# Kernel optimization log

Measured on AMD Instinct MI355X. Metric: run time of the kernel, lower is better.

The kernel has to match this reference:

```python
import jax, jax.numpy as jnp
import numpy as np

L = 16384          # leaves of complete binary tree
D = 256            # word_dim == tree_input_dim == output_dim
V = 50257          # num_words
NL = 5             # num_labels


def setup_inputs() -> dict:
    key = jax.random.key(0)
    ks = jax.random.split(key, 8)
    s = 0.05
    return {
        "tokens": jax.random.randint(ks[0], (L,), 0, V),
        "emb": jax.random.normal(ks[1], (V, D), jnp.float32) * s,      # word_embedding.weight
        "Wx": jax.random.normal(ks[2], (D, 5 * D), jnp.float32) * s,   # input->gates (leaf only)
        "Ul": jax.random.normal(ks[3], (D, 5 * D), jnp.float32) * s,   # left-child h -> gates
        "Ur": jax.random.normal(ks[4], (D, 5 * D), jnp.float32) * s,   # right-child h -> gates
        "b": jnp.zeros((5 * D,), jnp.float32),
        "Wp": jax.random.normal(ks[5], (D, NL), jnp.float32) * s,      # pred_layer
        "bp": jnp.zeros((NL,), jnp.float32),
    }


def _cell(pre, c_l, c_r):
    # Binary TreeLSTM cell: gates [i, f_l, f_r, o, u]
    i, fl, fr, o, u = jnp.split(pre, 5, axis=-1)
    c = jax.nn.sigmoid(i) * jnp.tanh(u) + jax.nn.sigmoid(fl) * c_l + jax.nn.sigmoid(fr) * c_r
    h = jax.nn.sigmoid(o) * jnp.tanh(c)
    return h, c


def reference(tokens, emb, Wx, Ul, Ur, b, Wp, bp):
    # dropout layers are identity at inference (no-op here)
    x = emb[tokens]                                  # [L, D] seq_output == word embeddings (leaf_rnn=False)
    # leaf nodes: l/r child states are zeros, inputs = seq_out[idx]
    h, c = _cell(x @ Wx + b, 0.0, 0.0)               # [L, D]
    hs = [h]
    # internal nodes level by level (complete binary tree): inputs=None -> no Wx term
    while h.shape[0] > 1:
        hl, hr = h[0::2], h[1::2]
        cl, cr = c[0::2], c[1::2]
        h, c = _cell(hl @ Ul + hr @ Ur + b, cl, cr)
        hs.append(h)
    hidden = jnp.concatenate(hs, axis=0)             # [2L-1, D] all node hidden states
    return hidden @ Wp + bp                          # single_h_pred logits [2L-1, NL]
```

## Files before the change

kernel.cpp:

```cpp
#include <hip/hip_runtime.h>
#include <hip/hip_bf16.h>
#include <math.h>
#include <stdint.h>


typedef __attribute__((ext_vector_type(8))) short     bf16x8;
typedef __attribute__((ext_vector_type(4))) float     f32x4;
typedef __attribute__((ext_vector_type(8))) unsigned short u16x8;

#define NGATE 5

__device__ __forceinline__ uint16_t f2bf(float f) {
    uint32_t u = __builtin_bit_cast(uint32_t, f);
    u = (u + 0x7fffu + ((u >> 16) & 1u)) >> 16;
    return (uint16_t)u;
}
__device__ __forceinline__ float bf2f(uint16_t h) {
    uint32_t u = ((uint32_t)h) << 16;
    return __builtin_bit_cast(float, u);
}
__device__ __forceinline__ float sigf(float x) { return 1.0f / (1.0f + __expf(-x)); }
__device__ __forceinline__ float tanhfast(float x) {
    float e = __expf(2.0f * x);
    return (e - 1.0f) / (e + 1.0f);
}

__device__ __forceinline__ void gld_lds16(const void* g, void* l) {
    __builtin_amdgcn_global_load_lds(
        (const __attribute__((address_space(1))) void*)g,
        (__attribute__((address_space(3))) void*)l,
        16, 0, 0);
}

__global__ __launch_bounds__(256) void pack_w_kernel(
    const float* __restrict__ W0, const float* __restrict__ W1, int KT,
    uint16_t* __restrict__ dhi, uint16_t* __restrict__ dlo)
{
    int gid = blockIdx.x * 256 + threadIdx.x;
    int total = 80 * KT * 64;
    if (gid >= total) return;
    int lane = gid & 63;
    int n  = ((gid >> 6) / KT) * 16 + (lane & 15);
    int kt = (gid >> 6) % KT;
    int k0 = kt * 32 + (lane >> 4) * 8;
    u16x8 vh, vl;
    #pragma unroll
    for (int j = 0; j < 8; ++j) {
        int k = k0 + j;
        const float* src = (k < 256) ? (W0 + (size_t)k * 1280)
                                     : (W1 + (size_t)(k - 256) * 1280);
        float v = src[n];
        uint16_t h = f2bf(v);
        vh[j] = h;
        vl[j] = f2bf(v - bf2f(h));
    }
    *(u16x8*)(dhi + (size_t)gid * 8) = vh;
    *(u16x8*)(dlo + (size_t)gid * 8) = vl;
}

template<int BM, int KT, bool LVL0>
__global__ __launch_bounds__(256) void lvl_gemm(
    const uint16_t* __restrict__ Ahi, const uint16_t* __restrict__ Alo,
    const int* __restrict__ tokens, const float* __restrict__ emb,
    const uint16_t* __restrict__ Bhi, const uint16_t* __restrict__ Blo,
    const float* __restrict__ b,
    const float* __restrict__ c_prev,
    uint16_t* __restrict__ h_hi_out, uint16_t* __restrict__ h_lo_out,
    float* __restrict__ c_out, int n)
{
    constexpr int K   = KT * 32;
    constexpr int MT  = BM / 64;
    constexpr int ACH = BM / 16;

    __shared__ __align__(16) uint16_t lA[2][BM * 32];
    __shared__ __align__(16) uint16_t lB[NGATE * 2 * 512];

    const int tid  = threadIdx.x;
    const int wave = tid >> 6;
    const int lane = tid & 63;
    const int quad = lane >> 4;
    const int l15  = lane & 15;
    const int r0   = blockIdx.x * BM;
    const int jn   = blockIdx.y;

    f32x4 acc[MT][NGATE] = {};

    for (int kt = 0; kt < KT; ++kt) {
        if (!LVL0) {
            for (int c = wave; c < 2 * ACH; c += 4) {
                int mat = (c >= ACH) ? 1 : 0;
                int ci  = mat ? (c - ACH) : c;
                const uint16_t* src = mat ? Alo : Ahi;
                int row = r0 + ci * 16 + (lane >> 2);
                row = min(row, n - 1);
                const uint16_t* g = src + (size_t)row * K + kt * 32 + (lane & 3) * 8;
                gld_lds16(g, &lA[mat][ci * 512]);
            }
        } else {
            int row = tid >> 1, kh = tid & 1;
            int tok = tokens[r0 + row];
            const float* src = emb + (size_t)tok * 256 + kt * 32 + kh * 16;
            float v[16];
            #pragma unroll
            for (int q = 0; q < 4; ++q) {
                float4 f = *(const float4*)(src + 4 * q);
                v[4*q] = f.x; v[4*q+1] = f.y; v[4*q+2] = f.z; v[4*q+3] = f.w;
            }
            u16x8 h0, h1, l0, l1;
            #pragma unroll
            for (int j = 0; j < 8; ++j) {
                uint16_t h = f2bf(v[j]);     h0[j] = h; l0[j] = f2bf(v[j]     - bf2f(h));
                uint16_t g = f2bf(v[j + 8]); h1[j] = g; l1[j] = f2bf(v[j + 8] - bf2f(g));
            }
            int o = row * 32 + kh * 16;
            *(u16x8*)&lA[0][o]     = h0;  *(u16x8*)&lA[0][o + 8] = h1;
            *(u16x8*)&lA[1][o]     = l0;  *(u16x8*)&lA[1][o + 8] = l1;
        }
        for (int c = wave; c < 2 * NGATE; c += 4) {
            int g  = c >> 1, hl = c & 1;
            const uint16_t* src = hl ? Blo : Bhi;
            int nt = g * 16 + jn;
            const uint16_t* gp = src + ((size_t)(nt * KT + kt) * 64 + lane) * 8;
            gld_lds16(gp, &lB[(g * 2 + hl) * 512]);
        }
        __syncthreads();

        bf16x8 a_hi[MT], a_lo[MT];
        #pragma unroll
        for (int mt = 0; mt < MT; ++mt) {
            int row = wave * (BM / 4) + mt * 16 + l15;
            a_hi[mt] = *(const bf16x8*)&lA[0][row * 32 + quad * 8];
            a_lo[mt] = *(const bf16x8*)&lA[1][row * 32 + quad * 8];
        }
        #pragma unroll
        for (int g = 0; g < NGATE; ++g) {
            bf16x8 bh = *(const bf16x8*)&lB[(g * 2 + 0) * 512 + lane * 8];
            bf16x8 bl = *(const bf16x8*)&lB[(g * 2 + 1) * 512 + lane * 8];
            #pragma unroll
            for (int mt = 0; mt < MT; ++mt) {
                acc[mt][g] = __builtin_amdgcn_mfma_f32_16x16x32_bf16(a_hi[mt], bh, acc[mt][g], 0, 0, 0);
                acc[mt][g] = __builtin_amdgcn_mfma_f32_16x16x32_bf16(a_lo[mt], bh, acc[mt][g], 0, 0, 0);
                acc[mt][g] = __builtin_amdgcn_mfma_f32_16x16x32_bf16(a_hi[mt], bl, acc[mt][g], 0, 0, 0);
            }
        }
        __syncthreads();
    }

    const int d = jn * 16 + l15;
    float bg[NGATE];
    #pragma unroll
    for (int g = 0; g < NGATE; ++g) bg[g] = b[g * 256 + d];

    #pragma unroll
    for (int mt = 0; mt < MT; ++mt) {
        int rb = r0 + wave * (BM / 4) + mt * 16 + quad * 4;
        #pragma unroll
        for (int v = 0; v < 4; ++v) {
            int row = rb + v;
            if (row < n) {
                float gi = acc[mt][0][v] + bg[0];
                float fl = acc[mt][1][v] + bg[1];
                float fr = acc[mt][2][v] + bg[2];
                float go = acc[mt][3][v] + bg[3];
                float gu = acc[mt][4][v] + bg[4];
                float cc;
                if (LVL0) {
                    cc = sigf(gi) * tanhfast(gu);
                } else {
                    float cl = c_prev[(size_t)(2 * row) * 256 + d];
                    float cr = c_prev[(size_t)(2 * row + 1) * 256 + d];
                    cc = sigf(gi) * tanhfast(gu) + sigf(fl) * cl + sigf(fr) * cr;
                }
                float hh = sigf(go) * tanhfast(cc);
                uint16_t hb = f2bf(hh);
                h_hi_out[(size_t)row * 256 + d] = hb;
                h_lo_out[(size_t)row * 256 + d] = f2bf(hh - bf2f(hb));
                c_out[(size_t)row * 256 + d] = cc;
            }
        }
    }
}

__global__ __launch_bounds__(256) void proj_kernel(
    const uint16_t* __restrict__ h_hi, const uint16_t* __restrict__ h_lo,
    const float* __restrict__ Wp, const float* __restrict__ bp,
    float* __restrict__ out, int n)
{
    const int wave = blockIdx.x * 4 + (threadIdx.x >> 6);
    const int lane = threadIdx.x & 63;
    if (wave >= n) return;

    const uint16_t* hh = h_hi + (size_t)wave * 256;
    const uint16_t* hl = h_lo + (size_t)wave * 256;
    float s[5] = {0.f, 0.f, 0.f, 0.f, 0.f};
    #pragma unroll
    for (int q = 0; q < 4; ++q) {
        int dd = lane + 64 * q;
        float hv = bf2f(hh[dd]) + bf2f(hl[dd]);
        #pragma unroll
        for (int j = 0; j < 5; ++j) s[j] += hv * Wp[dd * 5 + j];
    }
    #pragma unroll
    for (int off = 32; off; off >>= 1)
        #pragma unroll
        for (int j = 0; j < 5; ++j) s[j] += __shfl_down(s[j], off);

    if (lane == 0) {
        #pragma unroll
        for (int j = 0; j < 5; ++j) out[(size_t)wave * 5 + j] = s[j] + bp[j];
    }
}

extern "C" void kernel_launch(void* const* d_in, const int* in_sizes, int n_in,
                              void* d_out, int out_size, void* d_ws, size_t ws_size,
                              hipStream_t stream)
{
    const int*   tokens = (const int*)  d_in[0];
    const float* emb    = (const float*)d_in[1];
    const float* Wx     = (const float*)d_in[2];
    const float* Ul     = (const float*)d_in[3];
    const float* Ur     = (const float*)d_in[4];
    const float* b      = (const float*)d_in[5];
    const float* Wp     = (const float*)d_in[6];
    const float* bp     = (const float*)d_in[7];
    float* out = (float*)d_out;

    uint8_t* w = (uint8_t*)d_ws;
    uint16_t* h_hi = (uint16_t*)w;  w += (size_t)32767 * 256 * 2;
    uint16_t* h_lo = (uint16_t*)w;  w += (size_t)32767 * 256 * 2;
    float*    cA   = (float*)w;     w += (size_t)16384 * 256 * 4;
    float*    cB   = (float*)w;     w += (size_t)8192  * 256 * 4;
    uint16_t* BxH  = (uint16_t*)w;  w += (size_t)80 * 8  * 64 * 8 * 2;
    uint16_t* BxL  = (uint16_t*)w;  w += (size_t)80 * 8  * 64 * 8 * 2;
    uint16_t* BuH  = (uint16_t*)w;  w += (size_t)80 * 16 * 64 * 8 * 2;
    uint16_t* BuL  = (uint16_t*)w;  w += (size_t)80 * 16 * 64 * 8 * 2;

    pack_w_kernel<<<(80 * 8  * 64) / 256, 256, 0, stream>>>(Wx, Wx, 8,  BxH, BxL);
    pack_w_kernel<<<(80 * 16 * 64) / 256, 256, 0, stream>>>(Ul, Ur, 16, BuH, BuL);

    int off[16];
    off[0] = 0;
    for (int t = 0; t < 15; ++t) off[t + 1] = off[t] + (16384 >> t);

    lvl_gemm<128, 8, true><<<dim3(16384 / 128, 16), 256, 0, stream>>>(
        nullptr, nullptr, tokens, emb, BxH, BxL, b, nullptr,
        h_hi, h_lo, cA, 16384);

    for (int t = 1; t <= 14; ++t) {
        int n = 16384 >> t;
        const uint16_t* Ah = h_hi + (size_t)off[t - 1] * 256;
        const uint16_t* Al = h_lo + (size_t)off[t - 1] * 256;
        float* c_in  = (t % 2 == 0) ? cB : cA;
        float* c_out = (t % 2 == 0) ? cA : cB;
        uint16_t* Hh = h_hi + (size_t)off[t] * 256;
        uint16_t* Hl = h_lo + (size_t)off[t] * 256;
        if (n >= 4096) {
            lvl_gemm<128, 16, false><<<dim3(n / 128, 16), 256, 0, stream>>>(
                Ah, Al, nullptr, nullptr, BuH, BuL, b, c_in, Hh, Hl, c_out, n);
        } else {
            int gx = (n + 63) / 64; if (gx < 1) gx = 1;
            lvl_gemm<64, 16, false><<<dim3(gx, 16), 256, 0, stream>>>(
                Ah, Al, nullptr, nullptr, BuH, BuL, b, c_in, Hh, Hl, c_out, n);
        }
    }

    int total = off[15];
    proj_kernel<<<(total + 3) / 4, 256, 0, stream>>>(h_hi, h_lo, Wp, bp, out, total);
}
```

Measured before the change: 413.6 us.

## Rewrite TreeLSTM pipeline with MFMA-packed activations, fused projection, and single-block tail

Embeddings are gathered into a pre-packed MFMA fragment layout by a separate kernel. Each level's GEMM now reads A and B fragments directly from global memory instead of staging them through LDS with barriers. The epilogue scatters h straight into the next level's packed layout and fuses the 5-label projection through shuffle reductions and atomicAdds into a zeroed output. This removes the separate projection pass and the h hi/lo buffers. Levels 10–14 run in one 1024-thread block to cut launch overhead, at the cost of atomics, uncoalesced scatter stores and no LDS reuse of B.

```diff
diff --git a/kernel.cpp b/kernel.cpp
--- a/kernel.cpp
+++ b/kernel.cpp
@@ -1,14 +1,13 @@
 #include <hip/hip_runtime.h>
-#include <hip/hip_bf16.h>
 #include <math.h>
 #include <stdint.h>
 
 
-typedef __attribute__((ext_vector_type(8))) short     bf16x8;
-typedef __attribute__((ext_vector_type(4))) float     f32x4;
+typedef __attribute__((ext_vector_type(8))) short bf16x8;
+typedef __attribute__((ext_vector_type(4))) float f32x4;
 typedef __attribute__((ext_vector_type(8))) unsigned short u16x8;
 
-#define NGATE 5
+#define NG 5
 
 __device__ __forceinline__ uint16_t f2bf(float f) {
     uint32_t u = __builtin_bit_cast(uint32_t, f);
@@ -21,15 +20,34 @@
 }
 __device__ __forceinline__ float sigf(float x) { return 1.0f / (1.0f + __expf(-x)); }
 __device__ __forceinline__ float tanhfast(float x) {
+    x = fminf(fmaxf(x, -15.f), 15.f);
     float e = __expf(2.0f * x);
     return (e - 1.0f) / (e + 1.0f);
 }
 
-__device__ __forceinline__ void gld_lds16(const void* g, void* l) {
-    __builtin_amdgcn_global_load_lds(
-        (const __attribute__((address_space(1))) void*)g,
-        (__attribute__((address_space(3))) void*)l,
-        16, 0, 0);
+__global__ __launch_bounds__(256) void gather_emb(
+    const int* __restrict__ tokens, const float* __restrict__ emb,
+    uint16_t* __restrict__ A0)
+{
+    int W = blockIdx.x * 4 + (threadIdx.x >> 6);
+    int lane = threadIdx.x & 63;
+    int rt = W >> 3, kt = W & 7;
+    int m = lane & 15, q = lane >> 4;
+    int tok = tokens[rt * 16 + m];
+    const float* src = emb + (size_t)tok * 256 + kt * 32 + q * 8;
+    float4 f0 = *(const float4*)src;
+    float4 f1 = *(const float4*)(src + 4);
+    float v[8] = {f0.x, f0.y, f0.z, f0.w, f1.x, f1.y, f1.z, f1.w};
+    u16x8 hi, lo;
+    #pragma unroll
+    for (int j = 0; j < 8; ++j) {
+        uint16_t h = f2bf(v[j]);
+        hi[j] = h;
+        lo[j] = f2bf(v[j] - bf2f(h));
+    }
+    uint16_t* dst = A0 + (size_t)(rt * 8 + kt) * 1024;
+    *(u16x8*)(dst + lane * 8) = hi;
+    *(u16x8*)(dst + 512 + lane * 8) = lo;
 }
 
 __global__ __launch_bounds__(256) void pack_w_kernel(
@@ -58,156 +76,173 @@
     *(u16x8*)(dlo + (size_t)gid * 8) = vl;
 }
 
-template<int BM, int KT, bool LVL0>
-__global__ __launch_bounds__(256) void lvl_gemm(
-    const uint16_t* __restrict__ Ahi, const uint16_t* __restrict__ Alo,
-    const int* __restrict__ tokens, const float* __restrict__ emb,
-    const uint16_t* __restrict__ Bhi, const uint16_t* __restrict__ Blo,
-    const float* __restrict__ b,
-    const float* __restrict__ c_prev,
-    uint16_t* __restrict__ h_hi_out, uint16_t* __restrict__ h_lo_out,
-    float* __restrict__ c_out, int n)
-{
-    constexpr int K   = KT * 32;
-    constexpr int MT  = BM / 64;
-    constexpr int ACH = BM / 16;
-
-    __shared__ __align__(16) uint16_t lA[2][BM * 32];
-    __shared__ __align__(16) uint16_t lB[NGATE * 2 * 512];
-
-    const int tid  = threadIdx.x;
-    const int wave = tid >> 6;
-    const int lane = tid & 63;
-    const int quad = lane >> 4;
-    const int l15  = lane & 15;
-    const int r0   = blockIdx.x * BM;
-    const int jn   = blockIdx.y;
-
-    f32x4 acc[MT][NGATE] = {};
-
+__device__ __forceinline__ void do_row(
+    float gi, float fl, float fr, float go, float gu,
+    int row, int n, int d, int jn, bool lvl0,
+    const float* __restrict__ c_prev, uint16_t* __restrict__ A_out,
+    float* __restrict__ c_out, float* __restrict__ out,
+    const float* __restrict__ wp, const float* __restrict__ bp,
+    int write_next, int l15, int row_base)
+{
+    bool ok = row < n;
+    float h = 0.f;
+    if (ok) {
+        float cc;
+        if (lvl0) {
+            cc = sigf(gi) * tanhfast(gu);
+        } else {
+            float cl = c_prev[(size_t)(2 * row) * 256 + d];
+            float cr = c_prev[(size_t)(2 * row + 1) * 256 + d];
+            cc = sigf(gi) * tanhfast(gu) + sigf(fl) * cl + sigf(fr) * cr;
+        }
+        h = sigf(go) * tanhfast(cc);
+        if (write_next) {
+            c_out[(size_t)row * 256 + d] = cc;
+            int nrow = row >> 1;
+            int k = (row & 1) * 256 + d;
+            int kt = k >> 5, q2 = (k >> 3) & 3, j2 = k & 7;
+            int lane2 = (nrow & 15) + 16 * q2;
+            size_t base = (size_t)((nrow >> 4) * 16 + kt) * 1024 + lane2 * 8 + j2;
+            uint16_t hb = f2bf(h);
+            A_out[base] = hb;
+            A_out[base + 512] = f2bf(h - bf2f(hb));
+        }
+    }
+    float p[5];
+    #pragma unroll
+    for (int j = 0; j < 5; ++j) p[j] = h * wp[j];
+    #pragma unroll
+    for (int msk = 1; msk < 16; msk <<= 1) {
+        #pragma unroll
+        for (int j = 0; j < 5; ++j) p[j] += __shfl_xor(p[j], msk);
+    }
+    if (l15 == 0 && ok) {
+        #pragma unroll
+        for (int j = 0; j < 5; ++j) {
+            float add = p[j] + (jn == 0 ? bp[j] : 0.f);
+            atomicAdd(&out[(size_t)(row_base + row) * 5 + j], add);
+        }
+    }
+}
+
+template<int KT, int MT, bool LVL0>
+__global__ __launch_bounds__(256) void gemm_lvl(
+    const uint16_t* __restrict__ A,
+    const uint16_t* __restrict__ BH, const uint16_t* __restrict__ BL,
+    const float* __restrict__ bvec, const float* __restrict__ c_prev,
+    const float* __restrict__ Wp, const float* __restrict__ bp,
+    uint16_t* __restrict__ A_out, float* __restrict__ c_out,
+    float* __restrict__ out, int n, int write_next, int row_base)
+{
+    const int tid = threadIdx.x, wave = tid >> 6, lane = tid & 63;
+    const int quad = lane >> 4, l15 = lane & 15;
+    const int jn = blockIdx.y;
+    const int rw0 = (blockIdx.x * 4 + wave) * (16 * MT);
+    const int rowtiles = (n + 15) >> 4;
+
+    f32x4 acc[MT][NG] = {};
+
+    #pragma unroll 4
     for (int kt = 0; kt < KT; ++kt) {
-        if (!LVL0) {
-            for (int c = wave; c < 2 * ACH; c += 4) {
-                int mat = (c >= ACH) ? 1 : 0;
-                int ci  = mat ? (c - ACH) : c;
-                const uint16_t* src = mat ? Alo : Ahi;
-                int row = r0 + ci * 16 + (lane >> 2);
-                row = min(row, n - 1);
-                const uint16_t* g = src + (size_t)row * K + kt * 32 + (lane & 3) * 8;
-                gld_lds16(g, &lA[mat][ci * 512]);
-            }
-        } else {
-            int row = tid >> 1, kh = tid & 1;
-            int tok = tokens[r0 + row];
-            const float* src = emb + (size_t)tok * 256 + kt * 32 + kh * 16;
-            float v[16];
-            #pragma unroll
-            for (int q = 0; q < 4; ++q) {
-                float4 f = *(const float4*)(src + 4 * q);
-                v[4*q] = f.x; v[4*q+1] = f.y; v[4*q+2] = f.z; v[4*q+3] = f.w;
-            }
-            u16x8 h0, h1, l0, l1;
-            #pragma unroll
-            for (int j = 0; j < 8; ++j) {
-                uint16_t h = f2bf(v[j]);     h0[j] = h; l0[j] = f2bf(v[j]     - bf2f(h));
-                uint16_t g = f2bf(v[j + 8]); h1[j] = g; l1[j] = f2bf(v[j + 8] - bf2f(g));
-            }
-            int o = row * 32 + kh * 16;
-            *(u16x8*)&lA[0][o]     = h0;  *(u16x8*)&lA[0][o + 8] = h1;
-            *(u16x8*)&lA[1][o]     = l0;  *(u16x8*)&lA[1][o + 8] = l1;
-        }
-        for (int c = wave; c < 2 * NGATE; c += 4) {
-            int g  = c >> 1, hl = c & 1;
-            const uint16_t* src = hl ? Blo : Bhi;
-            int nt = g * 16 + jn;
-            const uint16_t* gp = src + ((size_t)(nt * KT + kt) * 64 + lane) * 8;
-            gld_lds16(gp, &lB[(g * 2 + hl) * 512]);
-        }
-        __syncthreads();
-
-        bf16x8 a_hi[MT], a_lo[MT];
+        bf16x8 ah[MT], al[MT];
         #pragma unroll
         for (int mt = 0; mt < MT; ++mt) {
-            int row = wave * (BM / 4) + mt * 16 + l15;
-            a_hi[mt] = *(const bf16x8*)&lA[0][row * 32 + quad * 8];
-            a_lo[mt] = *(const bf16x8*)&lA[1][row * 32 + quad * 8];
-        }
-        #pragma unroll
-        for (int g = 0; g < NGATE; ++g) {
-            bf16x8 bh = *(const bf16x8*)&lB[(g * 2 + 0) * 512 + lane * 8];
-            bf16x8 bl = *(const bf16x8*)&lB[(g * 2 + 1) * 512 + lane * 8];
+            int rt = rw0 / 16 + mt;
+            rt = min(rt, rowtiles - 1);
+            const uint16_t* at = A + (size_t)(rt * KT + kt) * 1024;
+            ah[mt] = *(const bf16x8*)(at + lane * 8);
+            al[mt] = *(const bf16x8*)(at + 512 + lane * 8);
+        }
+        #pragma unroll
+        for (int g = 0; g < NG; ++g) {
+            const size_t bo = (size_t)((g * 16 + jn) * KT + kt) * 512 + lane * 8;
+            bf16x8 bh = *(const bf16x8*)(BH + bo);
+            bf16x8 bl = *(const bf16x8*)(BL + bo);
             #pragma unroll
             for (int mt = 0; mt < MT; ++mt) {
-                acc[mt][g] = __builtin_amdgcn_mfma_f32_16x16x32_bf16(a_hi[mt], bh, acc[mt][g], 0, 0, 0);
-                acc[mt][g] = __builtin_amdgcn_mfma_f32_16x16x32_bf16(a_lo[mt], bh, acc[mt][g], 0, 0, 0);
-                acc[mt][g] = __builtin_amdgcn_mfma_f32_16x16x32_bf16(a_hi[mt], bl, acc[mt][g], 0, 0, 0);
+                acc[mt][g] = __builtin_amdgcn_mfma_f32_16x16x32_bf16(ah[mt], bh, acc[mt][g], 0, 0, 0);
+                acc[mt][g] = __builtin_amdgcn_mfma_f32_16x16x32_bf16(al[mt], bh, acc[mt][g], 0, 0, 0);
+                acc[mt][g] = __builtin_amdgcn_mfma_f32_16x16x32_bf16(ah[mt], bl, acc[mt][g], 0, 0, 0);
             }
         }
+    }
+
+    const int d = jn * 16 + l15;
+    float bg[NG], wp[5];
+    #pragma unroll
+    for (int g = 0; g < NG; ++g) bg[g] = bvec[g * 256 + d];
+    #pragma unroll
+    for (int j = 0; j < 5; ++j) wp[j] = Wp[d * 5 + j];
+
+    #pragma unroll
+    for (int mt = 0; mt < MT; ++mt) {
+        int rb = rw0 + mt * 16 + quad * 4;
+        #pragma unroll
+        for (int v = 0; v < 4; ++v) {
+            do_row(acc[mt][0][v] + bg[0], acc[mt][1][v] + bg[1],
+                   acc[mt][2][v] + bg[2], acc[mt][3][v] + bg[3],
+                   acc[mt][4][v] + bg[4],
+                   rb + v, n, d, jn, LVL0, c_prev, A_out, c_out, out,
+                   wp, bp, write_next, l15, row_base);
+        }
+    }
+}
+
+__global__ __launch_bounds__(1024) void tail_kernel(
+    uint16_t* __restrict__ AP0, uint16_t* __restrict__ AP1,
+    const uint16_t* __restrict__ BH, const uint16_t* __restrict__ BL,
+    const float* __restrict__ bvec, float* __restrict__ c0, float* __restrict__ c1,
+    const float* __restrict__ Wp, const float* __restrict__ bp,
+    float* __restrict__ out, int row_base10)
+{
+    const int tid = threadIdx.x, wave = tid >> 6, lane = tid & 63;
+    const int quad = lane >> 4, l15 = lane & 15;
+    const int jn = wave;
+    const int d = jn * 16 + l15;
+
+    float bg[NG], wp[5];
+    #pragma unroll
+    for (int g = 0; g < NG; ++g) bg[g] = bvec[g * 256 + d];
+    #pragma unroll
+    for (int j = 0; j < 5; ++j) wp[j] = Wp[d * 5 + j];
+
+    int row_base = row_base10;
+    for (int t = 10; t <= 14; ++t) {
+        int n = 16384 >> t;
+        const uint16_t* A = (t & 1) ? AP1 : AP0;
+        uint16_t* A_out   = (t & 1) ? AP0 : AP1;
+        const float* c_prev = (t & 1) ? c0 : c1;
+        float* c_out        = (t & 1) ? c1 : c0;
+        int write_next = (t < 14);
+
+        f32x4 acc[NG] = {};
+        #pragma unroll 4
+        for (int kt = 0; kt < 16; ++kt) {
+            const uint16_t* at = A + (size_t)kt * 1024;
+            bf16x8 ah = *(const bf16x8*)(at + lane * 8);
+            bf16x8 al = *(const bf16x8*)(at + 512 + lane * 8);
+            #pragma unroll
+            for (int g = 0; g < NG; ++g) {
+                const size_t bo = (size_t)((g * 16 + jn) * 16 + kt) * 512 + lane * 8;
+                bf16x8 bh = *(const bf16x8*)(BH + bo);
+                bf16x8 bl = *(const bf16x8*)(BL + bo);
+                acc[g] = __builtin_amdgcn_mfma_f32_16x16x32_bf16(ah, bh, acc[g], 0, 0, 0);
+                acc[g] = __builtin_amdgcn_mfma_f32_16x16x32_bf16(al, bh, acc[g], 0, 0, 0);
+                acc[g] = __builtin_amdgcn_mfma_f32_16x16x32_bf16(ah, bl, acc[g], 0, 0, 0);
+            }
+        }
+
+        int rb = quad * 4;
+        #pragma unroll
+        for (int v = 0; v < 4; ++v) {
+            do_row(acc[0][v] + bg[0], acc[1][v] + bg[1], acc[2][v] + bg[2],
+                   acc[3][v] + bg[3], acc[4][v] + bg[4],
+                   rb + v, n, d, jn, false, c_prev, A_out, c_out, out,
+                   wp, bp, write_next, l15, row_base);
+        }
+        row_base += n;
+        __threadfence();
         __syncthreads();
-    }
-
-    const int d = jn * 16 + l15;
-    float bg[NGATE];
-    #pragma unroll
-    for (int g = 0; g < NGATE; ++g) bg[g] = b[g * 256 + d];
-
-    #pragma unroll
-    for (int mt = 0; mt < MT; ++mt) {
-        int rb = r0 + wave * (BM / 4) + mt * 16 + quad * 4;
-        #pragma unroll
-        for (int v = 0; v < 4; ++v) {
-            int row = rb + v;
-            if (row < n) {
-                float gi = acc[mt][0][v] + bg[0];
-                float fl = acc[mt][1][v] + bg[1];
-                float fr = acc[mt][2][v] + bg[2];
-                float go = acc[mt][3][v] + bg[3];
-                float gu = acc[mt][4][v] + bg[4];
-                float cc;
-                if (LVL0) {
-                    cc = sigf(gi) * tanhfast(gu);
-                } else {
-                    float cl = c_prev[(size_t)(2 * row) * 256 + d];
-                    float cr = c_prev[(size_t)(2 * row + 1) * 256 + d];
-                    cc = sigf(gi) * tanhfast(gu) + sigf(fl) * cl + sigf(fr) * cr;
-                }
-                float hh = sigf(go) * tanhfast(cc);
-                uint16_t hb = f2bf(hh);
-                h_hi_out[(size_t)row * 256 + d] = hb;
-                h_lo_out[(size_t)row * 256 + d] = f2bf(hh - bf2f(hb));
-                c_out[(size_t)row * 256 + d] = cc;
-            }
-        }
-    }
-}
-
-__global__ __launch_bounds__(256) void proj_kernel(
-    const uint16_t* __restrict__ h_hi, const uint16_t* __restrict__ h_lo,
-    const float* __restrict__ Wp, const float* __restrict__ bp,
-    float* __restrict__ out, int n)
-{
-    const int wave = blockIdx.x * 4 + (threadIdx.x >> 6);
-    const int lane = threadIdx.x & 63;
-    if (wave >= n) return;
-
-    const uint16_t* hh = h_hi + (size_t)wave * 256;
-    const uint16_t* hl = h_lo + (size_t)wave * 256;
-    float s[5] = {0.f, 0.f, 0.f, 0.f, 0.f};
-    #pragma unroll
-    for (int q = 0; q < 4; ++q) {
-        int dd = lane + 64 * q;
-        float hv = bf2f(hh[dd]) + bf2f(hl[dd]);
-        #pragma unroll
-        for (int j = 0; j < 5; ++j) s[j] += hv * Wp[dd * 5 + j];
-    }
-    #pragma unroll
-    for (int off = 32; off; off >>= 1)
-        #pragma unroll
-        for (int j = 0; j < 5; ++j) s[j] += __shfl_down(s[j], off);
-
-    if (lane == 0) {
-        #pragma unroll
-        for (int j = 0; j < 5; ++j) out[(size_t)wave * 5 + j] = s[j] + bp[j];
     }
 }
 
@@ -226,44 +261,40 @@
     float* out = (float*)d_out;
 
     uint8_t* w = (uint8_t*)d_ws;
-    uint16_t* h_hi = (uint16_t*)w;  w += (size_t)32767 * 256 * 2;
-    uint16_t* h_lo = (uint16_t*)w;  w += (size_t)32767 * 256 * 2;
-    float*    cA   = (float*)w;     w += (size_t)16384 * 256 * 4;
-    float*    cB   = (float*)w;     w += (size_t)8192  * 256 * 4;
-    uint16_t* BxH  = (uint16_t*)w;  w += (size_t)80 * 8  * 64 * 8 * 2;
-    uint16_t* BxL  = (uint16_t*)w;  w += (size_t)80 * 8  * 64 * 8 * 2;
-    uint16_t* BuH  = (uint16_t*)w;  w += (size_t)80 * 16 * 64 * 8 * 2;
-    uint16_t* BuL  = (uint16_t*)w;  w += (size_t)80 * 16 * 64 * 8 * 2;
-
-    pack_w_kernel<<<(80 * 8  * 64) / 256, 256, 0, stream>>>(Wx, Wx, 8,  BxH, BxL);
-    pack_w_kernel<<<(80 * 16 * 64) / 256, 256, 0, stream>>>(Ul, Ur, 16, BuH, BuL);
+    uint16_t* AP0 = (uint16_t*)w;  w += (size_t)1024 * 8  * 1024 * 2;
+    uint16_t* AP1 = (uint16_t*)w;  w += (size_t)512  * 16 * 1024 * 2;
+    float*    c0  = (float*)w;     w += (size_t)16384 * 256 * 4;
+    float*    c1  = (float*)w;     w += (size_t)8192  * 256 * 4;
+    uint16_t* BxH = (uint16_t*)w;  w += (size_t)80 * 8  * 512 * 2;
+    uint16_t* BxL = (uint16_t*)w;  w += (size_t)80 * 8  * 512 * 2;
+    uint16_t* BuH = (uint16_t*)w;  w += (size_t)80 * 16 * 512 * 2;
+    uint16_t* BuL = (uint16_t*)w;  w += (size_t)80 * 16 * 512 * 2;
+
+    hipMemsetAsync(out, 0, (size_t)32767 * 5 * sizeof(float), stream);
+
+    gather_emb<<<2048, 256, 0, stream>>>(tokens, emb, AP0);
+    pack_w_kernel<<<160, 256, 0, stream>>>(Wx, Wx, 8,  BxH, BxL);
+    pack_w_kernel<<<320, 256, 0, stream>>>(Ul, Ur, 16, BuH, BuL);
 
     int off[16];
     off[0] = 0;
     for (int t = 0; t < 15; ++t) off[t + 1] = off[t] + (16384 >> t);
 
-    lvl_gemm<128, 8, true><<<dim3(16384 / 128, 16), 256, 0, stream>>>(
-        nullptr, nullptr, tokens, emb, BxH, BxL, b, nullptr,
-        h_hi, h_lo, cA, 16384);
-
-    for (int t = 1; t <= 14; ++t) {
+    gemm_lvl<8, 2, true><<<dim3(128, 16), 256, 0, stream>>>(
+        AP0, BxH, BxL, b, nullptr, Wp, bp, AP1, c0, out, 16384, 1, 0);
+
+    for (int t = 1; t <= 3; ++t) {
         int n = 16384 >> t;
-        const uint16_t* Ah = h_hi + (size_t)off[t - 1] * 256;
-        const uint16_t* Al = h_lo + (size_t)off[t - 1] * 256;
-        float* c_in  = (t % 2 == 0) ? cB : cA;
-        float* c_out = (t % 2 == 0) ? cA : cB;
-        uint16_t* Hh = h_hi + (size_t)off[t] * 256;
-        uint16_t* Hl = h_lo + (size_t)off[t] * 256;
-        if (n >= 4096) {
-            lvl_gemm<128, 16, false><<<dim3(n / 128, 16), 256, 0, stream>>>(
-                Ah, Al, nullptr, nullptr, BuH, BuL, b, c_in, Hh, Hl, c_out, n);
-        } else {
-            int gx = (n + 63) / 64; if (gx < 1) gx = 1;
-            lvl_gemm<64, 16, false><<<dim3(gx, 16), 256, 0, stream>>>(
-                Ah, Al, nullptr, nullptr, BuH, BuL, b, c_in, Hh, Hl, c_out, n);
-        }
-    }
-
-    int total = off[15];
-    proj_kernel<<<(total + 3) / 4, 256, 0, stream>>>(h_hi, h_lo, Wp, bp, out, total);
-}
+        gemm_lvl<16, 2, false><<<dim3(n / 128, 16), 256, 0, stream>>>(
+            (t & 1) ? AP1 : AP0, BuH, BuL, b, (t & 1) ? c0 : c1, Wp, bp,
+            (t & 1) ? AP0 : AP1, (t & 1) ? c1 : c0, out, n, 1, off[t]);
+    }
+    for (int t = 4; t <= 9; ++t) {
+        int n = 16384 >> t;
+        int gx = (n + 63) / 64;
+        gemm_lvl<16, 1, false><<<dim3(gx, 16), 256, 0, stream>>>(
+            (t & 1) ? AP1 : AP0, BuH, BuL, b, (t & 1) ? c0 : c1, Wp, bp,
+            (t & 1) ? AP0 : AP1, (t & 1) ? c1 : c0, out, n, 1, off[t]);
+    }
+    tail_kernel<<<1, 1024, 0, stream>>>(AP0, AP1, BuH, BuL, b, c0, c1, Wp, bp, out, off[10]);
+}
```

Measured after the change: 638.8 us. +54.5%, slower.
